# Performance work log

Measured on AMD Instinct MI355X. Metric: run time of the kernel, lower is better.

Reference implementation:

```python
import jax, jax.numpy as jnp
import numpy as np

B, T, H, E, V = 64, 512, 512, 128, 2048  # batch, seq, hidden_dim, embedding_dim, label_size


def setup_inputs() -> dict:
    key = jax.random.key(0)
    ks = jax.random.split(key, 10)
    s = 0.02
    return {
        "encoder_outputs": jax.random.normal(ks[0], (B, T, H), dtype=jnp.float32),
        "input_mask": jnp.ones((B, T), dtype=jnp.int32),
        "emb_table": jax.random.normal(ks[1], (V, E), dtype=jnp.float32) * s,
        "W_ih": jax.random.normal(ks[2], (4 * H, E + 2 * H), dtype=jnp.float32) * s,
        "b_ih": jnp.zeros((4 * H,), dtype=jnp.float32),
        "b_hh": jnp.zeros((4 * H,), dtype=jnp.float32),
        "W_attn": jax.random.normal(ks[3], (H, H), dtype=jnp.float32) * s,
        "b_attn": jnp.zeros((H,), dtype=jnp.float32),
        "W_out": jax.random.normal(ks[4], (V, 2 * H), dtype=jnp.float32) * s,
        "b_out": jnp.zeros((V,), dtype=jnp.float32),
    }


def reference(encoder_outputs, input_mask, emb_table, W_ih, b_ih, b_hh,
              W_attn, b_attn, W_out, b_out):
    # Faithful translation of NMTDecoder.forward_model (returns per-step
    # log-softmax scores [B, T, V]; the original .forward() takes argmax(-1)).
    enc = encoder_outputs                     # [B, T, H]
    b, t, h = enc.shape
    neg_mask = (input_mask == 0)              # [B, T] positions masked in attention

    # initial context: encoder output at real_length - 1 per batch element
    lengths = jnp.sum(input_mask, axis=1)
    ctx0 = enc[jnp.arange(b), lengths - 1]    # [B, H]
    emb0 = jnp.zeros((b, emb_table.shape[1]), dtype=enc.dtype)  # [B, E]

    # attn Linear only depends on encoder_outputs -> precompute once
    energies = jnp.einsum('bth,kh->btk', enc, W_attn) + b_attn  # [B, T, H]

    bias = b_ih + b_hh  # LSTM restarted from zero state every step, so h0=c0=0

    def step(carry, enc_t):
        embedded, context = carry             # [B,E], [B,H]
        x = jnp.concatenate([embedded, context, enc_t], axis=-1)  # [B, E+2H]
        gates = x @ W_ih.T + bias             # [B, 4H], pytorch gate order i,f,g,o
        i_g, f_g, g_g, o_g = jnp.split(gates, 4, axis=-1)
        c = jax.nn.sigmoid(i_g) * jnp.tanh(g_g)      # f*c0 = 0
        hdn = jax.nn.sigmoid(o_g) * jnp.tanh(c)      # [B, H]

        score = jnp.concatenate([hdn, context], axis=-1) @ W_out.T + b_out  # [B, V]
        logp = jax.nn.log_softmax(score, axis=-1)
        pred = jnp.argmax(logp, axis=-1)             # greedy feed-back
        emb_next = emb_table[pred]                   # [B, E]

        attn_logits = jnp.einsum('btk,bk->bt', energies, hdn)
        attn_logits = jnp.where(neg_mask, jnp.float32(-1e12), attn_logits)
        alpha = jax.nn.softmax(attn_logits, axis=-1)
        ctx_next = jnp.einsum('bt,bth->bh', alpha, enc)
        return (emb_next, ctx_next), logp

    _, logps = jax.lax.scan(step, (emb0, ctx0), jnp.swapaxes(enc, 0, 1))
    return jnp.swapaxes(logps, 0, 1)  # [B, T, V]
```

## Files before the change

### kernel.cpp

```cpp
#include <hip/hip_runtime.h>
#include <cstddef>
#include <cstdint>
#include <cmath>

#define NBLK 256
#define NTHR 512

#define L_WIH   0
#define L_WOUT  6912
#define L_WT    15104
#define L_VVS   16128
#define L_FA    16640
#define L_TOT   33024

#define WS_HDN   64
#define WS_VV    32832
#define WS_SC    65600
#define WS_PACC  196672
#define WS_PS    262208
#define WS_EMB   262336

__device__ __forceinline__ float dot4(float4 a, float4 b) {
    return a.x*b.x + a.y*b.y + a.z*b.z + a.w*b.w;
}

__device__ __forceinline__ void st1(float* p, float v) {
    __hip_atomic_store(p, v, __ATOMIC_RELAXED, __HIP_MEMORY_SCOPE_AGENT);
}
__device__ __forceinline__ void st2(float* p, float a, float b) {
    union { unsigned long long u; float2 f; } c; c.f = make_float2(a, b);
    __hip_atomic_store((unsigned long long*)p, c.u,
        __ATOMIC_RELAXED, __HIP_MEMORY_SCOPE_AGENT);
}

__device__ __forceinline__ void gridbar(unsigned* cnt, unsigned* gen, unsigned iter) {
    asm volatile("s_waitcnt vmcnt(0) lgkmcnt(0)" ::: "memory");
    __syncthreads();
    if (threadIdx.x == 0) {
        unsigned prev = __hip_atomic_fetch_add(cnt, 1u, __ATOMIC_RELAXED,
                                               __HIP_MEMORY_SCOPE_AGENT);
        if (prev == iter * NBLK - 1u) {
            __hip_atomic_store(gen, iter, __ATOMIC_RELAXED, __HIP_MEMORY_SCOPE_AGENT);
        } else {
            while (__hip_atomic_load(gen, __ATOMIC_RELAXED, __HIP_MEMORY_SCOPE_AGENT) < iter)
                __builtin_amdgcn_s_sleep(2);
        }
    }
    __syncthreads();
    (void)__hip_atomic_load(gen, __ATOMIC_ACQUIRE, __HIP_MEMORY_SCOPE_AGENT);
    asm volatile("" ::: "memory");
}

__global__ __launch_bounds__(NTHR, 1) void nmt_fused(
    const float* __restrict__ enc, const int* __restrict__ mask,
    const float* __restrict__ embTab, const float* __restrict__ Wih,
    const float* __restrict__ bih, const float* __restrict__ bhh,
    const float* __restrict__ Wa, const float* __restrict__ Wout,
    const float* __restrict__ bout, float* __restrict__ out,
    float* __restrict__ ws)
{
    extern __shared__ float smem[];

    const int blk = blockIdx.x;
    const int tid = threadIdx.x;

    unsigned* cnt = (unsigned*)ws;
    unsigned* gen = (unsigned*)ws + 32;
    float* hdnw = ws + WS_HDN;
    float* vvw  = ws + WS_VV;
    float* scw  = ws + WS_SC;
    float* pacc = ws + WS_PACC;
    float* ps   = ws + WS_PS;
    float* embw = ws + WS_EMB;

    unsigned bar = 0;

    {
        #pragma unroll
        for (int s = 0; s < 6; ++s) {
            const int grow = (s < 2) ? (2 * blk + s)
                           : (s < 4) ? (1024 + 2 * blk + (s - 2))
                                     : (1536 + 2 * blk + (s - 4));
            for (int off = tid; off < 1152; off += NTHR)
                smem[L_WIH + s * 1152 + off] = Wih[(size_t)grow * 1152 + off];
        }
        #pragma unroll
        for (int s = 0; s < 8; ++s)
            for (int off = tid; off < 1024; off += NTHR)
                smem[L_WOUT + s * 1024 + off] = Wout[(size_t)(8 * blk + s) * 1024 + off];
        #pragma unroll
        for (int s = 0; s < 2; ++s)
            smem[L_WT + s * 512 + tid] = Wa[(size_t)tid * 512 + (2 * blk + s)];
    }
    const int c0 = 2 * blk;
    const float bi0 = bih[c0]        + bhh[c0];
    const float bi1 = bih[c0 + 1]    + bhh[c0 + 1];
    const float bg0 = bih[1024 + c0] + bhh[1024 + c0];
    const float bg1 = bih[1025 + c0] + bhh[1025 + c0];
    const float bo0 = bih[1536 + c0] + bhh[1536 + c0];
    const float bo1 = bih[1537 + c0] + bhh[1537 + c0];
    float bo[8];
    #pragma unroll
    for (int s = 0; s < 8; ++s) bo[s] = bout[8 * blk + s];

    if (blk < 64) {
        const int b = blk;
        int* ism = (int*)(smem + L_FA);
        ism[tid] = mask[b * 512 + tid];
        __syncthreads();
        for (int off = 256; off; off >>= 1) {
            if (tid < off) ism[tid] += ism[tid + off];
            __syncthreads();
        }
        int tl = ism[0] - 1;
        if (tl < 0) tl = 0;
        st1(pacc + 32768 + b * 512 + tid, enc[((size_t)(b * 512 + tl)) * 512 + tid]);
        if (tid == 0) st1(ps + 64 + b, 1.f);
        if (tid < 128) st1(embw + b * 128 + tid, 0.f);
    }
    gridbar(cnt, gen, ++bar);

    for (int t = 0; t < 512; ++t) {
        const int cur = t & 1;
        float* paccC = pacc + cur * 32768;
        const float* paccP = pacc + (cur ^ 1) * 32768;
        float* psC = ps + cur * 64;
        const float* psP = ps + (cur ^ 1) * 64;

        {
            if (tid < 128) st1(paccC + blk * 128 + tid, 0.f);
            if (blk == 0 && tid < 64) st1(psC + tid, 0.f);

            const int q = tid & 15, bl = tid >> 4;
            #pragma unroll
            for (int pass = 0; pass < 2; ++pass) {
                const int b = pass * 32 + bl;
                float sden = psP[b];
                float inv = (sden != 0.f) ? 1.f / sden : 0.f;

                float4 x[18];
                const float* embb = embw + b * 128;
                x[0] = *(const float4*)(embb + q * 8);
                x[1] = *(const float4*)(embb + q * 8 + 4);
                const float* pb = paccP + b * 512;
                #pragma unroll
                for (int c = 0; c < 4; ++c) {
                    float4 p0 = *(const float4*)(pb + c * 128 + q * 8);
                    float4 p1 = *(const float4*)(pb + c * 128 + q * 8 + 4);
                    x[2 + c * 2] = make_float4(p0.x * inv, p0.y * inv, p0.z * inv, p0.w * inv);
                    x[3 + c * 2] = make_float4(p1.x * inv, p1.y * inv, p1.z * inv, p1.w * inv);
                }
                const float* eb = enc + ((size_t)(b * 512 + t)) * 512;
                #pragma unroll
                for (int c = 0; c < 4; ++c) {
                    x[10 + c * 2] = *(const float4*)(eb + c * 128 + q * 8);
                    x[11 + c * 2] = *(const float4*)(eb + c * 128 + q * 8 + 4);
                }

                float acc[6];
                #pragma unroll
                for (int s = 0; s < 6; ++s) {
                    const float* wl = smem + L_WIH + s * 1152 + q * 8;
                    float a = 0.f;
                    #pragma unroll
                    for (int c = 0; c < 9; ++c) {
                        a += dot4(*(const float4*)(wl + c * 128),     x[c * 2]);
                        a += dot4(*(const float4*)(wl + c * 128 + 4), x[c * 2 + 1]);
                    }
                    acc[s] = a;
                }
                #pragma unroll
                for (int s = 0; s < 6; ++s) {
                    #pragma unroll
                    for (int off = 1; off < 16; off <<= 1)
                        acc[s] += __shfl_xor(acc[s], off);
                }
                if (q == 0) {
                    float ig0 = acc[0] + bi0, ig1 = acc[1] + bi1;
                    float gg0 = acc[2] + bg0, gg1 = acc[3] + bg1;
                    float og0 = acc[4] + bo0, og1 = acc[5] + bo1;
                    float cv0 = (1.f / (1.f + expf(-ig0))) * tanhf(gg0);
                    float cv1 = (1.f / (1.f + expf(-ig1))) * tanhf(gg1);
                    float h0 = (1.f / (1.f + expf(-og0))) * tanhf(cv0);
                    float h1 = (1.f / (1.f + expf(-og1))) * tanhf(cv1);
                    st2(hdnw + b * 512 + c0, h0, h1);
                }
            }
        }
        gridbar(cnt, gen, ++bar);

        {
            const int q = tid & 15, bl = tid >> 4;
            #pragma unroll
            for (int pass = 0; pass < 2; ++pass) {
                const int b = pass * 32 + bl;
                float sden = psP[b];
                float inv = (sden != 0.f) ? 1.f / sden : 0.f;

                float4 x[16];
                const float* hb = hdnw + b * 512;
                #pragma unroll
                for (int c = 0; c < 4; ++c) {
                    x[c * 2]     = *(const float4*)(hb + c * 128 + q * 8);
                    x[c * 2 + 1] = *(const float4*)(hb + c * 128 + q * 8 + 4);
                }
                const float* pb = paccP + b * 512;
                #pragma unroll
                for (int c = 0; c < 4; ++c) {
                    float4 p0 = *(const float4*)(pb + c * 128 + q * 8);
                    float4 p1 = *(const float4*)(pb + c * 128 + q * 8 + 4);
                    x[8 + c * 2] = make_float4(p0.x * inv, p0.y * inv, p0.z * inv, p0.w * inv);
                    x[9 + c * 2] = make_float4(p1.x * inv, p1.y * inv, p1.z * inv, p1.w * inv);
                }

                float acc[8];
                #pragma unroll
                for (int s = 0; s < 8; ++s) {
                    const float* wl = smem + L_WOUT + s * 1024 + q * 8;
                    float a = 0.f;
                    #pragma unroll
                    for (int c = 0; c < 8; ++c) {
                        a += dot4(*(const float4*)(wl + c * 128),     x[c * 2]);
                        a += dot4(*(const float4*)(wl + c * 128 + 4), x[c * 2 + 1]);
                    }
                    acc[s] = a;
                }
                float av[2];
                #pragma unroll
                for (int s = 0; s < 2; ++s) {
                    const float* wl = smem + L_WT + s * 512 + q * 8;
                    float a = 0.f;
                    #pragma unroll
                    for (int c = 0; c < 4; ++c) {
                        a += dot4(*(const float4*)(wl + c * 128),     x[c * 2]);
                        a += dot4(*(const float4*)(wl + c * 128 + 4), x[c * 2 + 1]);
                    }
                    av[s] = a;
                }
                #pragma unroll
                for (int s = 0; s < 8; ++s) {
                    #pragma unroll
                    for (int off = 1; off < 16; off <<= 1)
                        acc[s] += __shfl_xor(acc[s], off);
                }
                #pragma unroll
                for (int s = 0; s < 2; ++s) {
                    #pragma unroll
                    for (int off = 1; off < 16; off <<= 1)
                        av[s] += __shfl_xor(av[s], off);
                }
                if (q == 0) {
                    float sv0 = acc[0] + bo[0], sv1 = acc[1] + bo[1];
                    float sv2 = acc[2] + bo[2], sv3 = acc[3] + bo[3];
                    float sv4 = acc[4] + bo[4], sv5 = acc[5] + bo[5];
                    float sv6 = acc[6] + bo[6], sv7 = acc[7] + bo[7];
                    float* sb = scw + b * 2048 + 8 * blk;
                    st2(sb,     sv0, sv1);
                    st2(sb + 2, sv2, sv3);
                    st2(sb + 4, sv4, sv5);
                    st2(sb + 6, sv6, sv7);
                    st2(vvw + b * 512 + c0, av[0], av[1]);
                }
            }
        }
        gridbar(cnt, gen, ++bar);

        {
            const int fb = blk >> 2, r = blk & 3;
            float* fa = smem + L_FA;
            int* fai = (int*)(fa + 512);

            if (tid < 256) {
                float2 v = *(const float2*)(vvw + fb * 512 + tid * 2);
                *(float2*)(smem + L_VVS + tid * 2) = v;
            }

            const float* sb = scw + fb * 2048;
            float sv[4];
            float bv = -3.4e38f; int bi = 0;
            #pragma unroll
            for (int jj = 0; jj < 4; ++jj) {
                const int c = tid + (jj << 9);
                sv[jj] = sb[c];
                if (sv[jj] > bv) { bv = sv[jj]; bi = c; }
            }
            fa[tid] = bv; fai[tid] = bi;
            __syncthreads();
            for (int off = 256; off; off >>= 1) {
                if (tid < off) {
                    float ov = fa[tid + off]; int oi = fai[tid + off];
                    if (ov > fa[tid] || (ov == fa[tid] && oi < fai[tid])) {
                        fa[tid] = ov; fai[tid] = oi;
                    }
                }
                __syncthreads();
            }
            const float gmax = fa[0];
            const int amax = fai[0];
            __syncthreads();
            float psum = 0.f;
            #pragma unroll
            for (int jj = 0; jj < 4; ++jj) psum += expf(sv[jj] - gmax);
            fa[tid] = psum;
            __syncthreads();
            for (int off = 256; off; off >>= 1) {
                if (tid < off) fa[tid] += fa[tid + off];
                __syncthreads();
            }
            const float lse = gmax + logf(fa[0]);

            {
                float v = ((r == 0) ? sv[0] : (r == 1) ? sv[1] : (r == 2) ? sv[2] : sv[3]) - lse;
                st1(out + ((size_t)(fb * 512 + t)) * 2048 + r * 512 + tid, v);
            }
            if (r == 0 && tid < 64) {
                const float* er = embTab + (size_t)amax * 128 + tid * 2;
                st2(embw + fb * 128 + tid * 2, er[0], er[1]);
            }

            const int w = tid >> 6, lane = tid & 63, l = lane & 15, g = lane >> 4;
            float4 v4[8];
            #pragma unroll
            for (int j = 0; j < 8; ++j)
                v4[j] = *(const float4*)(smem + L_VVS + l * 32 + j * 4);

            float4 a4[8];
            #pragma unroll
            for (int j = 0; j < 8; ++j) a4[j] = make_float4(0.f, 0.f, 0.f, 0.f);
            float s_loc = 0.f;
            for (int p = 0; p < 4; ++p) {
                const int ta = r * 128 + p * 32 + w * 4 + g;
                const int mk = mask[fb * 512 + ta];
                const float* er = enc + ((size_t)(fb * 512 + ta)) * 512 + l * 32;
                float4 e4[8];
                #pragma unroll
                for (int j = 0; j < 8; ++j) e4[j] = *(const float4*)(er + j * 4);
                float d = 0.f;
                #pragma unroll
                for (int j = 0; j < 8; ++j) d += dot4(e4[j], v4[j]);
                d += __shfl_xor(d, 1);
                d += __shfl_xor(d, 2);
                d += __shfl_xor(d, 4);
                d += __shfl_xor(d, 8);
                const float pw = mk ? expf(d) : 0.f;
                s_loc += pw;
                #pragma unroll
                for (int j = 0; j < 8; ++j) {
                    a4[j].x += pw * e4[j].x; a4[j].y += pw * e4[j].y;
                    a4[j].z += pw * e4[j].z; a4[j].w += pw * e4[j].w;
                }
            }
            __syncthreads();
            {
                float* row = fa + (w * 4 + g) * 512 + l * 32;
                #pragma unroll
                for (int j = 0; j < 8; ++j)
                    ((float4*)row)[(j + l) & 7] = a4[j];
            }
            __syncthreads();
            {
                const int lh = tid >> 5, jh = (tid >> 2) & 7, comp = tid & 3;
                const int off0 = lh * 32 + ((jh + lh) & 7) * 4 + comp;
                float a = 0.f;
                #pragma unroll
                for (int R = 0; R < 32; ++R) a += fa[R * 512 + off0];
                atomicAdd(paccC + fb * 512 + tid, a);
            }
            __syncthreads();
            if (l == 0) fa[w * 4 + g] = s_loc;
            __syncthreads();
            if (tid == 0) {
                float s = 0.f;
                #pragma unroll
                for (int R = 0; R < 32; ++R) s += fa[R];
                atomicAdd(psC + fb, s);
            }
        }
        gridbar(cnt, gen, ++bar);
    }
}

extern "C" void kernel_launch(void* const* d_in, const int* in_sizes, int n_in,
                              void* d_out, int out_size, void* d_ws, size_t ws_size,
                              hipStream_t stream)
{
    const float* enc    = (const float*)d_in[0];
    const int*   mask   = (const int*)  d_in[1];
    const float* embTab = (const float*)d_in[2];
    const float* Wih    = (const float*)d_in[3];
    const float* bih    = (const float*)d_in[4];
    const float* bhh    = (const float*)d_in[5];
    const float* Wa     = (const float*)d_in[6];
    const float* Wout   = (const float*)d_in[8];
    const float* bout   = (const float*)d_in[9];
    float* out = (float*)d_out;
    float* wsf = (float*)d_ws;

    (void)hipFuncSetAttribute((const void*)nmt_fused,
                              hipFuncAttributeMaxDynamicSharedMemorySize, 163840);

    hipMemsetAsync(d_ws, 0, 256, stream);

    void* args[] = {
        (void*)&enc, (void*)&mask, (void*)&embTab, (void*)&Wih, (void*)&bih,
        (void*)&bhh, (void*)&Wa, (void*)&Wout, (void*)&bout, (void*)&out,
        (void*)&wsf
    };
    hipLaunchCooperativeKernel((void*)nmt_fused, dim3(NBLK), dim3(NTHR),
                               args, (unsigned)(L_TOT * sizeof(float)), stream);
}
```

Before: 47.95 ms.

## Hierarchical grid barrier, batch-blocked GEMVs, and partial softmax/argmax reduction

Replaces the flat grid barrier with a two-level barrier: groups of 8 blocks count locally before one representative touches the global counter. This reduces contention on a single atomic. The LSTM-gate and output projections are restructured so each thread processes 4 batch rows per smem weight load, improving weight reuse. The output-projection blocks now emit per-block max, sum-exp and argmax partials, so the final phase merges 256 partials instead of rescanning all 2048 logits with block-wide tree reductions. It also changes launch bounds to allow 2 blocks per CU, at some register-pressure risk.

New measurement: 62.90 ms. 1.31x slower.

```diff
diff --git a/kernel.cpp b/kernel.cpp
--- a/kernel.cpp
+++ b/kernel.cpp
@@ -10,15 +10,17 @@
 #define L_WOUT  6912
 #define L_WT    15104
 #define L_VVS   16128
-#define L_FA    16640
-#define L_TOT   33024
-
-#define WS_HDN   64
-#define WS_VV    32832
-#define WS_SC    65600
-#define WS_PACC  196672
-#define WS_PS    262208
-#define WS_EMB   262336
+#define L_FA    16768
+#define L_TOT   33152
+
+#define WS_BAR   0
+#define WS_HDN   1088
+#define WS_VV    33856
+#define WS_SC    66624
+#define WS_PACC  197696
+#define WS_PS    263232
+#define WS_EMB   263360
+#define WS_PART  271552
 
 __device__ __forceinline__ float dot4(float4 a, float4 b) {
     return a.x*b.x + a.y*b.y + a.z*b.z + a.w*b.w;
@@ -33,25 +35,30 @@
         __ATOMIC_RELAXED, __HIP_MEMORY_SCOPE_AGENT);
 }
 
-__device__ __forceinline__ void gridbar(unsigned* cnt, unsigned* gen, unsigned iter) {
+__device__ __forceinline__ void gridbar(unsigned* bar, unsigned iter) {
     asm volatile("s_waitcnt vmcnt(0) lgkmcnt(0)" ::: "memory");
     __syncthreads();
     if (threadIdx.x == 0) {
-        unsigned prev = __hip_atomic_fetch_add(cnt, 1u, __ATOMIC_RELAXED,
-                                               __HIP_MEMORY_SCOPE_AGENT);
-        if (prev == iter * NBLK - 1u) {
-            __hip_atomic_store(gen, iter, __ATOMIC_RELAXED, __HIP_MEMORY_SCOPE_AGENT);
-        } else {
-            while (__hip_atomic_load(gen, __ATOMIC_RELAXED, __HIP_MEMORY_SCOPE_AGENT) < iter)
-                __builtin_amdgcn_s_sleep(2);
-        }
+        const unsigned g = blockIdx.x >> 3;
+        unsigned p = __hip_atomic_fetch_add(bar + 64 + g * 32, 1u,
+                        __ATOMIC_RELAXED, __HIP_MEMORY_SCOPE_AGENT);
+        if (p == iter * 8u - 1u) {
+            unsigned rp = __hip_atomic_fetch_add(bar, 1u,
+                        __ATOMIC_RELAXED, __HIP_MEMORY_SCOPE_AGENT);
+            if (rp == iter * 32u - 1u)
+                __hip_atomic_store(bar + 32, iter, __ATOMIC_RELAXED,
+                                   __HIP_MEMORY_SCOPE_AGENT);
+        }
+        while (__hip_atomic_load(bar + 32, __ATOMIC_RELAXED,
+                                 __HIP_MEMORY_SCOPE_AGENT) < iter)
+            __builtin_amdgcn_s_sleep(1);
     }
     __syncthreads();
-    (void)__hip_atomic_load(gen, __ATOMIC_ACQUIRE, __HIP_MEMORY_SCOPE_AGENT);
+    (void)__hip_atomic_load(bar + 32, __ATOMIC_ACQUIRE, __HIP_MEMORY_SCOPE_AGENT);
     asm volatile("" ::: "memory");
 }
 
-__global__ __launch_bounds__(NTHR, 1) void nmt_fused(
+__global__ __launch_bounds__(NTHR, 2) void nmt_fused(
     const float* __restrict__ enc, const int* __restrict__ mask,
     const float* __restrict__ embTab, const float* __restrict__ Wih,
     const float* __restrict__ bih, const float* __restrict__ bhh,
@@ -64,23 +71,23 @@
     const int blk = blockIdx.x;
     const int tid = threadIdx.x;
 
-    unsigned* cnt = (unsigned*)ws;
-    unsigned* gen = (unsigned*)ws + 32;
+    unsigned* bar = (unsigned*)ws;
     float* hdnw = ws + WS_HDN;
     float* vvw  = ws + WS_VV;
     float* scw  = ws + WS_SC;
     float* pacc = ws + WS_PACC;
     float* ps   = ws + WS_PS;
     float* embw = ws + WS_EMB;
-
-    unsigned bar = 0;
+    float* partw= ws + WS_PART;
+
+    unsigned bi = 0;
 
     {
         #pragma unroll
         for (int s = 0; s < 6; ++s) {
-            const int grow = (s < 2) ? (2 * blk + s)
-                           : (s < 4) ? (1024 + 2 * blk + (s - 2))
-                                     : (1536 + 2 * blk + (s - 4));
+            const int sh = s / 3, gate = s % 3;
+            const int col = 2 * blk + sh;
+            const int grow = (gate == 0) ? col : (gate == 1) ? 1024 + col : 1536 + col;
             for (int off = tid; off < 1152; off += NTHR)
                 smem[L_WIH + s * 1152 + off] = Wih[(size_t)grow * 1152 + off];
         }
@@ -92,16 +99,18 @@
         for (int s = 0; s < 2; ++s)
             smem[L_WT + s * 512 + tid] = Wa[(size_t)tid * 512 + (2 * blk + s)];
     }
-    const int c0 = 2 * blk;
-    const float bi0 = bih[c0]        + bhh[c0];
-    const float bi1 = bih[c0 + 1]    + bhh[c0 + 1];
-    const float bg0 = bih[1024 + c0] + bhh[1024 + c0];
-    const float bg1 = bih[1025 + c0] + bhh[1025 + c0];
-    const float bo0 = bih[1536 + c0] + bhh[1536 + c0];
-    const float bo1 = bih[1537 + c0] + bhh[1537 + c0];
-    float bo[8];
+    const int q  = tid & 15;
+    const int rh = (tid >> 4) & 1;
+    const int bl = tid >> 5;
+    const int hi = (q >> 3) & 1;
+
+    const int colP1 = 2 * blk + rh;
+    const float biB = bih[colP1]        + bhh[colP1];
+    const float bgB = bih[1024 + colP1] + bhh[1024 + colP1];
+    const float boB = bih[1536 + colP1] + bhh[1536 + colP1];
+    float bo_r[4];
     #pragma unroll
-    for (int s = 0; s < 8; ++s) bo[s] = bout[8 * blk + s];
+    for (int rr = 0; rr < 4; ++rr) bo_r[rr] = bout[8 * blk + rh * 4 + rr];
 
     if (blk < 64) {
         const int b = blk;
@@ -118,7 +127,7 @@
         if (tid == 0) st1(ps + 64 + b, 1.f);
         if (tid < 128) st1(embw + b * 128 + tid, 0.f);
     }
-    gridbar(cnt, gen, ++bar);
+    gridbar(bar, ++bi);
 
     for (int t = 0; t < 512; ++t) {
         const int cur = t & 1;
@@ -131,186 +140,215 @@
             if (tid < 128) st1(paccC + blk * 128 + tid, 0.f);
             if (blk == 0 && tid < 64) st1(psC + tid, 0.f);
 
-            const int q = tid & 15, bl = tid >> 4;
-            #pragma unroll
-            for (int pass = 0; pass < 2; ++pass) {
-                const int b = pass * 32 + bl;
-                float sden = psP[b];
-                float inv = (sden != 0.f) ? 1.f / sden : 0.f;
-
-                float4 x[18];
-                const float* embb = embw + b * 128;
-                x[0] = *(const float4*)(embb + q * 8);
-                x[1] = *(const float4*)(embb + q * 8 + 4);
-                const float* pb = paccP + b * 512;
-                #pragma unroll
-                for (int c = 0; c < 4; ++c) {
-                    float4 p0 = *(const float4*)(pb + c * 128 + q * 8);
-                    float4 p1 = *(const float4*)(pb + c * 128 + q * 8 + 4);
-                    x[2 + c * 2] = make_float4(p0.x * inv, p0.y * inv, p0.z * inv, p0.w * inv);
-                    x[3 + c * 2] = make_float4(p1.x * inv, p1.y * inv, p1.z * inv, p1.w * inv);
-                }
-                const float* eb = enc + ((size_t)(b * 512 + t)) * 512;
-                #pragma unroll
-                for (int c = 0; c < 4; ++c) {
-                    x[10 + c * 2] = *(const float4*)(eb + c * 128 + q * 8);
-                    x[11 + c * 2] = *(const float4*)(eb + c * 128 + q * 8 + 4);
-                }
-
-                float acc[6];
-                #pragma unroll
-                for (int s = 0; s < 6; ++s) {
-                    const float* wl = smem + L_WIH + s * 1152 + q * 8;
-                    float a = 0.f;
+            float invs[4];
+            #pragma unroll
+            for (int i = 0; i < 4; ++i) {
+                float sden = psP[4 * bl + i];
+                invs[i] = (sden != 0.f) ? 1.f / sden : 0.f;
+            }
+
+            float acc[3][4];
+            #pragma unroll
+            for (int gq = 0; gq < 3; ++gq)
+                #pragma unroll
+                for (int i = 0; i < 4; ++i) acc[gq][i] = 0.f;
+
+            #pragma unroll
+            for (int c = 0; c < 9; ++c) {
+                float4 xA[4], xB[4];
+                #pragma unroll
+                for (int i = 0; i < 4; ++i) {
+                    const int b = 4 * bl + i;
+                    const float* src;
+                    if (c == 0)      src = embw + b * 128 + q * 8;
+                    else if (c <= 4) src = paccP + b * 512 + (c - 1) * 128 + q * 8;
+                    else             src = enc + ((size_t)(b * 512 + t)) * 512
+                                               + (c - 5) * 128 + q * 8;
+                    float4 a = *(const float4*)(src + 4 * hi);
+                    float4 bq = *(const float4*)(src + 4 - 4 * hi);
+                    if (c >= 1 && c <= 4) {
+                        const float sc_ = invs[i];
+                        a.x *= sc_; a.y *= sc_; a.z *= sc_; a.w *= sc_;
+                        bq.x *= sc_; bq.y *= sc_; bq.z *= sc_; bq.w *= sc_;
+                    }
+                    xA[i] = a; xB[i] = bq;
+                }
+                #pragma unroll
+                for (int gq = 0; gq < 3; ++gq) {
+                    const float* wl = smem + L_WIH + (rh * 3 + gq) * 1152
+                                    + c * 128 + q * 8;
+                    float4 w0 = *(const float4*)(wl + 4 * hi);
+                    float4 w1 = *(const float4*)(wl + 4 - 4 * hi);
                     #pragma unroll
-                    for (int c = 0; c < 9; ++c) {
-                        a += dot4(*(const float4*)(wl + c * 128),     x[c * 2]);
-                        a += dot4(*(const float4*)(wl + c * 128 + 4), x[c * 2 + 1]);
-                    }
-                    acc[s] = a;
-                }
-                #pragma unroll
-                for (int s = 0; s < 6; ++s) {
+                    for (int i = 0; i < 4; ++i)
+                        acc[gq][i] += dot4(w0, xA[i]) + dot4(w1, xB[i]);
+                }
+            }
+            #pragma unroll
+            for (int gq = 0; gq < 3; ++gq)
+                #pragma unroll
+                for (int i = 0; i < 4; ++i) {
                     #pragma unroll
                     for (int off = 1; off < 16; off <<= 1)
-                        acc[s] += __shfl_xor(acc[s], off);
-                }
-                if (q == 0) {
-                    float ig0 = acc[0] + bi0, ig1 = acc[1] + bi1;
-                    float gg0 = acc[2] + bg0, gg1 = acc[3] + bg1;
-                    float og0 = acc[4] + bo0, og1 = acc[5] + bo1;
-                    float cv0 = (1.f / (1.f + expf(-ig0))) * tanhf(gg0);
-                    float cv1 = (1.f / (1.f + expf(-ig1))) * tanhf(gg1);
-                    float h0 = (1.f / (1.f + expf(-og0))) * tanhf(cv0);
-                    float h1 = (1.f / (1.f + expf(-og1))) * tanhf(cv1);
-                    st2(hdnw + b * 512 + c0, h0, h1);
-                }
-            }
-        }
-        gridbar(cnt, gen, ++bar);
+                        acc[gq][i] += __shfl_xor(acc[gq][i], off);
+                }
+            if (q == 0) {
+                #pragma unroll
+                for (int i = 0; i < 4; ++i) {
+                    const int b = 4 * bl + i;
+                    float ig = acc[0][i] + biB;
+                    float gg = acc[1][i] + bgB;
+                    float og = acc[2][i] + boB;
+                    float cv = (1.f / (1.f + expf(-ig))) * tanhf(gg);
+                    float hv = (1.f / (1.f + expf(-og))) * tanhf(cv);
+                    st1(hdnw + b * 512 + colP1, hv);
+                }
+            }
+        }
+        gridbar(bar, ++bi);
 
         {
-            const int q = tid & 15, bl = tid >> 4;
-            #pragma unroll
-            for (int pass = 0; pass < 2; ++pass) {
-                const int b = pass * 32 + bl;
-                float sden = psP[b];
-                float inv = (sden != 0.f) ? 1.f / sden : 0.f;
-
-                float4 x[16];
-                const float* hb = hdnw + b * 512;
-                #pragma unroll
-                for (int c = 0; c < 4; ++c) {
-                    x[c * 2]     = *(const float4*)(hb + c * 128 + q * 8);
-                    x[c * 2 + 1] = *(const float4*)(hb + c * 128 + q * 8 + 4);
-                }
-                const float* pb = paccP + b * 512;
-                #pragma unroll
-                for (int c = 0; c < 4; ++c) {
-                    float4 p0 = *(const float4*)(pb + c * 128 + q * 8);
-                    float4 p1 = *(const float4*)(pb + c * 128 + q * 8 + 4);
-                    x[8 + c * 2] = make_float4(p0.x * inv, p0.y * inv, p0.z * inv, p0.w * inv);
-                    x[9 + c * 2] = make_float4(p1.x * inv, p1.y * inv, p1.z * inv, p1.w * inv);
-                }
-
-                float acc[8];
-                #pragma unroll
-                for (int s = 0; s < 8; ++s) {
-                    const float* wl = smem + L_WOUT + s * 1024 + q * 8;
-                    float a = 0.f;
+            float invs[4];
+            #pragma unroll
+            for (int i = 0; i < 4; ++i) {
+                float sden = psP[4 * bl + i];
+                invs[i] = (sden != 0.f) ? 1.f / sden : 0.f;
+            }
+
+            float acc_s[4][4], acc_v[4];
+            #pragma unroll
+            for (int rr = 0; rr < 4; ++rr)
+                #pragma unroll
+                for (int i = 0; i < 4; ++i) acc_s[rr][i] = 0.f;
+            #pragma unroll
+            for (int i = 0; i < 4; ++i) acc_v[i] = 0.f;
+
+            #pragma unroll
+            for (int c = 0; c < 8; ++c) {
+                float4 xA[4], xB[4];
+                #pragma unroll
+                for (int i = 0; i < 4; ++i) {
+                    const int b = 4 * bl + i;
+                    const float* src = (c < 4)
+                        ? (hdnw + b * 512 + c * 128 + q * 8)
+                        : (paccP + b * 512 + (c - 4) * 128 + q * 8);
+                    float4 a = *(const float4*)(src + 4 * hi);
+                    float4 bq = *(const float4*)(src + 4 - 4 * hi);
+                    if (c >= 4) {
+                        const float sc_ = invs[i];
+                        a.x *= sc_; a.y *= sc_; a.z *= sc_; a.w *= sc_;
+                        bq.x *= sc_; bq.y *= sc_; bq.z *= sc_; bq.w *= sc_;
+                    }
+                    xA[i] = a; xB[i] = bq;
+                }
+                #pragma unroll
+                for (int rr = 0; rr < 4; ++rr) {
+                    const float* wl = smem + L_WOUT + (rh * 4 + rr) * 1024
+                                    + c * 128 + q * 8;
+                    float4 w0 = *(const float4*)(wl + 4 * hi);
+                    float4 w1 = *(const float4*)(wl + 4 - 4 * hi);
                     #pragma unroll
-                    for (int c = 0; c < 8; ++c) {
-                        a += dot4(*(const float4*)(wl + c * 128),     x[c * 2]);
-                        a += dot4(*(const float4*)(wl + c * 128 + 4), x[c * 2 + 1]);
-                    }
-                    acc[s] = a;
-                }
-                float av[2];
-                #pragma unroll
-                for (int s = 0; s < 2; ++s) {
-                    const float* wl = smem + L_WT + s * 512 + q * 8;
-                    float a = 0.f;
+                    for (int i = 0; i < 4; ++i)
+                        acc_s[rr][i] += dot4(w0, xA[i]) + dot4(w1, xB[i]);
+                }
+                if (c < 4) {
+                    const float* wl = smem + L_WT + rh * 512 + c * 128 + q * 8;
+                    float4 w0 = *(const float4*)(wl + 4 * hi);
+                    float4 w1 = *(const float4*)(wl + 4 - 4 * hi);
                     #pragma unroll
-                    for (int c = 0; c < 4; ++c) {
-                        a += dot4(*(const float4*)(wl + c * 128),     x[c * 2]);
-                        a += dot4(*(const float4*)(wl + c * 128 + 4), x[c * 2 + 1]);
-                    }
-                    av[s] = a;
-                }
-                #pragma unroll
-                for (int s = 0; s < 8; ++s) {
+                    for (int i = 0; i < 4; ++i)
+                        acc_v[i] += dot4(w0, xA[i]) + dot4(w1, xB[i]);
+                }
+            }
+            #pragma unroll
+            for (int rr = 0; rr < 4; ++rr)
+                #pragma unroll
+                for (int i = 0; i < 4; ++i) {
                     #pragma unroll
                     for (int off = 1; off < 16; off <<= 1)
-                        acc[s] += __shfl_xor(acc[s], off);
-                }
-                #pragma unroll
-                for (int s = 0; s < 2; ++s) {
-                    #pragma unroll
-                    for (int off = 1; off < 16; off <<= 1)
-                        av[s] += __shfl_xor(av[s], off);
-                }
-                if (q == 0) {
-                    float sv0 = acc[0] + bo[0], sv1 = acc[1] + bo[1];
-                    float sv2 = acc[2] + bo[2], sv3 = acc[3] + bo[3];
-                    float sv4 = acc[4] + bo[4], sv5 = acc[5] + bo[5];
-                    float sv6 = acc[6] + bo[6], sv7 = acc[7] + bo[7];
-                    float* sb = scw + b * 2048 + 8 * blk;
-                    st2(sb,     sv0, sv1);
-                    st2(sb + 2, sv2, sv3);
-                    st2(sb + 4, sv4, sv5);
-                    st2(sb + 6, sv6, sv7);
-                    st2(vvw + b * 512 + c0, av[0], av[1]);
-                }
-            }
-        }
-        gridbar(cnt, gen, ++bar);
+                        acc_s[rr][i] += __shfl_xor(acc_s[rr][i], off);
+                }
+            #pragma unroll
+            for (int i = 0; i < 4; ++i) {
+                #pragma unroll
+                for (int off = 1; off < 16; off <<= 1)
+                    acc_v[i] += __shfl_xor(acc_v[i], off);
+            }
+            if (q == 0) {
+                #pragma unroll
+                for (int i = 0; i < 4; ++i) {
+                    const int b = 4 * bl + i;
+                    float s0 = acc_s[0][i] + bo_r[0];
+                    float s1 = acc_s[1][i] + bo_r[1];
+                    float s2 = acc_s[2][i] + bo_r[2];
+                    float s3 = acc_s[3][i] + bo_r[3];
+                    float* sb = scw + b * 2048 + 8 * blk + rh * 4;
+                    st2(sb, s0, s1); st2(sb + 2, s2, s3);
+                    st1(vvw + b * 512 + 2 * blk + rh, acc_v[i]);
+                    float m4 = s0; int i4 = 0;
+                    if (s1 > m4) { m4 = s1; i4 = 1; }
+                    if (s2 > m4) { m4 = s2; i4 = 2; }
+                    if (s3 > m4) { m4 = s3; i4 = 3; }
+                    int gidx = 8 * blk + rh * 4 + i4;
+                    float se4 = expf(s0 - m4) + expf(s1 - m4)
+                              + expf(s2 - m4) + expf(s3 - m4);
+                    float mo  = __shfl_xor(m4, 16);
+                    float seo = __shfl_xor(se4, 16);
+                    int   io  = __shfl_xor(gidx, 16);
+                    float M = fmaxf(m4, mo);
+                    float se = se4 * expf(m4 - M) + seo * expf(mo - M);
+                    int idx = (mo > m4 || (mo == m4 && io < gidx)) ? io : gidx;
+                    if (rh == 0) {
+                        float* pp = partw + ((size_t)b * 256 + blk) * 4;
+                        st2(pp, M, se);
+                        st2(pp + 2, (float)idx, 0.f);
+                    }
+                }
+            }
+        }
+        gridbar(bar, ++bi);
 
         {
             const int fb = blk >> 2, r = blk & 3;
-            float* fa = smem + L_FA;
-            int* fai = (int*)(fa + 512);
 
             if (tid < 256) {
                 float2 v = *(const float2*)(vvw + fb * 512 + tid * 2);
                 *(float2*)(smem + L_VVS + tid * 2) = v;
             }
-
-            const float* sb = scw + fb * 2048;
-            float sv[4];
-            float bv = -3.4e38f; int bi = 0;
-            #pragma unroll
-            for (int jj = 0; jj < 4; ++jj) {
-                const int c = tid + (jj << 9);
-                sv[jj] = sb[c];
-                if (sv[jj] > bv) { bv = sv[jj]; bi = c; }
-            }
-            fa[tid] = bv; fai[tid] = bi;
-            __syncthreads();
-            for (int off = 256; off; off >>= 1) {
-                if (tid < off) {
-                    float ov = fa[tid + off]; int oi = fai[tid + off];
-                    if (ov > fa[tid] || (ov == fa[tid] && oi < fai[tid])) {
-                        fa[tid] = ov; fai[tid] = oi;
-                    }
-                }
-                __syncthreads();
-            }
-            const float gmax = fa[0];
-            const int amax = fai[0];
-            __syncthreads();
-            float psum = 0.f;
-            #pragma unroll
-            for (int jj = 0; jj < 4; ++jj) psum += expf(sv[jj] - gmax);
-            fa[tid] = psum;
-            __syncthreads();
-            for (int off = 256; off; off >>= 1) {
-                if (tid < off) fa[tid] += fa[tid + off];
-                __syncthreads();
-            }
-            const float lse = gmax + logf(fa[0]);
+            if (tid < 64) {
+                float m = -3.4e38f, se = 0.f; int idx = 0x7fffffff;
+                #pragma unroll
+                for (int kk = 0; kk < 4; ++kk) {
+                    const float* pp = partw + ((size_t)fb * 256 + tid + kk * 64) * 4;
+                    float2 a = *(const float2*)pp;
+                    float2 ci = *(const float2*)(pp + 2);
+                    float M = fmaxf(m, a.x);
+                    se = se * expf(m - M) + a.y * expf(a.x - M);
+                    int i2 = (int)ci.x;
+                    idx = (a.x > m || (a.x == m && i2 < idx)) ? i2 : idx;
+                    m = M;
+                }
+                #pragma unroll
+                for (int off = 1; off < 64; off <<= 1) {
+                    float mo = __shfl_xor(m, off);
+                    float seo = __shfl_xor(se, off);
+                    int io = __shfl_xor(idx, off);
+                    float M = fmaxf(m, mo);
+                    se = se * expf(m - M) + seo * expf(mo - M);
+                    idx = (mo > m || (mo == m && io < idx)) ? io : idx;
+                    m = M;
+                }
+                if (tid == 0) {
+                    smem[L_VVS + 512] = m + logf(se);
+                    smem[L_VVS + 513] = (float)idx;
+                }
+            }
+            __syncthreads();
+            const float lse = smem[L_VVS + 512];
+            const int amax = (int)smem[L_VVS + 513];
 
             {
-                float v = ((r == 0) ? sv[0] : (r == 1) ? sv[1] : (r == 2) ? sv[2] : sv[3]) - lse;
+                float v = scw[fb * 2048 + r * 512 + tid] - lse;
                 st1(out + ((size_t)(fb * 512 + t)) * 2048 + r * 512 + tid, v);
             }
             if (r == 0 && tid < 64) {
@@ -350,6 +388,7 @@
                     a4[j].z += pw * e4[j].z; a4[j].w += pw * e4[j].w;
                 }
             }
+            float* fa = smem + L_FA;
             __syncthreads();
             {
                 float* row = fa + (w * 4 + g) * 512 + l * 32;
@@ -376,7 +415,7 @@
                 atomicAdd(psC + fb, s);
             }
         }
-        gridbar(cnt, gen, ++bar);
+        gridbar(bar, ++bi);
     }
 }
 
@@ -399,7 +438,7 @@
     (void)hipFuncSetAttribute((const void*)nmt_fused,
                               hipFuncAttributeMaxDynamicSharedMemorySize, 163840);
 
-    hipMemsetAsync(d_ws, 0, 256, stream);
+    hipMemsetAsync(d_ws, 0, 4352, stream);
 
     void* args[] = {
         (void*)&enc, (void*)&mask, (void*)&embTab, (void*)&Wih, (void*)&bih,
```
